# Kernel optimization log

Measured on AMD Instinct MI355X. Metric: run time of the kernel, lower is better.

Reference implementation:

```python
import jax, jax.numpy as jnp
import numpy as np

POLY_DEGREE = 2
EPS = 1e-10
MAX_INTER = 25

# Upper-triangle index pairs (i<j) in the same row-major order as the
# original double loop: (0,1),(0,2),...,(0,24),(1,2),...
_IU0, _IU1 = np.triu_indices(MAX_INTER, k=1)


def setup_inputs() -> dict:
    key = jax.random.key(0)
    x = jax.random.normal(key, (524288, 25), dtype=jnp.float32)
    return {"x": x}


def reference(x) -> jnp.ndarray:
    feats = [x]
    # polynomial features: degrees 2..POLY_DEGREE
    for degree in range(2, POLY_DEGREE + 1):
        feats.append(jnp.power(x, degree))
    ax = jnp.abs(x) + EPS
    feats.append(jnp.log(ax))            # log features
    feats.append(jnp.sqrt(ax))           # sqrt features
    feats.append(jnp.power(ax, 1.0 / 3.0))  # cbrt features
    # pairwise interactions among first min(F,25) columns, upper triangle
    inter = x[:, _IU0] * x[:, _IU1]      # [B, 300]
    feats.append(inter)
    return jnp.concatenate(feats, axis=1)  # [B, 400]
```

## Files before the change

### kernel.cpp

```cpp
#include <hip/hip_runtime.h>

#define NF     25
#define NPAIR  300
#define NUNARY 125
#define NCOL   425
#define ROWS   8
#define BLK    256
#define TILE_DW (ROWS * NCOL)
#define TILE4   (TILE_DW / 4)
#define VALS_N  (ROWS * NF + ROWS * NUNARY + 4)

typedef float f32x4 __attribute__((ext_vector_type(4)));
typedef unsigned int u32;
typedef u32 u32x4 __attribute__((ext_vector_type(4)));

#define ONE_SLOT (ROWS * NF + ROWS * NUNARY)

__global__ __launch_bounds__(BLK) void feat_expand_kernel(
    const float* __restrict__ x, float* __restrict__ out,
    int nrows, int nchunks) {
  __shared__ float vals[VALS_N];
  __shared__ u32x4 dtab4[TILE4];
  u32* dtab = (u32*)dtab4;

  const int tid = threadIdx.x;
  const int r200 = tid / NF;
  const int i200 = tid - r200 * NF;

  if (tid == 0) vals[ONE_SLOT] = 1.0f;
  for (int o = tid; o < TILE_DW; o += BLK) {
    const int r = o / NCOL, c = o - r * NCOL;
    u32 d;
    if (c < NUNARY) {
      d = (u32)(ROWS * NF + r * NUNARY + c) | ((u32)ONE_SLOT << 16);
    } else {
      int rem = c - NUNARY, i = 0;
      while (rem >= (NF - 1 - i)) { rem -= (NF - 1 - i); ++i; }
      const int j = i + 1 + rem;
      d = (u32)(r * NF + i) | ((u32)(r * NF + j) << 16);
    }
    dtab[o] = d;
  }

  for (int chunk = blockIdx.x; chunk < nchunks; chunk += gridDim.x) {
    const long long rowbase = (long long)chunk * ROWS;
    const long long remrows = nrows - rowbase;
    const int rows_here = (int)(remrows < ROWS ? remrows : ROWS);

    __syncthreads();

    if (tid < ROWS * NF && r200 < rows_here) {
      const float v = x[rowbase * NF + tid];
      vals[tid] = v;
      float* ur = &vals[ROWS * NF + r200 * NUNARY];
      const float ax = fabsf(v) + 1e-10f;
      const float l2 = __builtin_amdgcn_logf(ax);
      ur[i200]          = v;
      ur[NF + i200]     = v * v;
      ur[2*NF + i200]   = l2 * 0.69314718055994530942f;
      ur[3*NF + i200]   = sqrtf(ax);
      ur[4*NF + i200]   = __builtin_amdgcn_exp2f(l2 * (1.0f/3.0f));
    }
    __syncthreads();

    if (rows_here == ROWS) {
      f32x4* __restrict__ o4 = (f32x4*)(out + rowbase * NCOL);
#pragma unroll
      for (int k = 0; k < 4; ++k) {
        const int v4 = tid + k * BLK;
        if (k < 3 || v4 < TILE4) {
          const u32x4 d = dtab4[v4];
          f32x4 ov;
          ov.x = vals[d.x & 0xFFFF] * vals[d.x >> 16];
          ov.y = vals[d.y & 0xFFFF] * vals[d.y >> 16];
          ov.z = vals[d.z & 0xFFFF] * vals[d.z >> 16];
          ov.w = vals[d.w & 0xFFFF] * vals[d.w >> 16];
          __builtin_nontemporal_store(ov, &o4[v4]);
        }
      }
    } else {
      const int total = rows_here * NCOL;
      for (int o = tid; o < total; o += BLK) {
        const u32 d = dtab[o];
        out[rowbase * NCOL + o] = vals[d & 0xFFFF] * vals[d >> 16];
      }
    }
  }
}

extern "C" void kernel_launch(void* const* d_in, const int* in_sizes, int n_in,
                              void* d_out, int out_size, void* d_ws, size_t ws_size,
                              hipStream_t stream) {
  const float* x = (const float*)d_in[0];
  float* out = (float*)d_out;

  const int nrows = in_sizes[0] / NF;
  const int nchunks = (nrows + ROWS - 1) / ROWS;
  const int grid = nchunks < 4096 ? nchunks : 4096;

  feat_expand_kernel<<<grid, BLK, 0, stream>>>(x, out, nrows, nchunks);
}
```

Baseline: 214.7 us.

## Give each wavefront its own 4-row chunk to drop block-wide barriers

Each 64-lane wavefront now processes its own 4-row chunk, with a private region of shared memory for input and unary values. Because no data is shared across wavefronts, the two per-iteration __syncthreads are removed and only one barrier remains after the lookup table is built. The aim is to let wavefronts run independently and hide memory latency without block-wide stalls. Correctness now relies on lockstep execution within a wavefront for the shared-memory store-then-load, with no explicit wave barrier. Each wavefront also does fewer stores per input load.

```diff
diff --git a/kernel.cpp b/kernel.cpp
--- a/kernel.cpp
+++ b/kernel.cpp
@@ -1,88 +1,92 @@
 #include <hip/hip_runtime.h>
 
 #define NF     25
-#define NPAIR  300
 #define NUNARY 125
 #define NCOL   425
-#define ROWS   8
+#define WROWS  4
 #define BLK    256
-#define TILE_DW (ROWS * NCOL)
+#define WAVES  (BLK / 64)
+#define WXS    (WROWS * NF)
+#define WVALS  608
+#define ONE_OFF 600
+#define TILE_DW (WROWS * NCOL)
 #define TILE4   (TILE_DW / 4)
-#define VALS_N  (ROWS * NF + ROWS * NUNARY + 4)
 
 typedef float f32x4 __attribute__((ext_vector_type(4)));
 typedef unsigned int u32;
 typedef u32 u32x4 __attribute__((ext_vector_type(4)));
 
-#define ONE_SLOT (ROWS * NF + ROWS * NUNARY)
-
 __global__ __launch_bounds__(BLK) void feat_expand_kernel(
     const float* __restrict__ x, float* __restrict__ out,
-    int nrows, int nchunks) {
-  __shared__ float vals[VALS_N];
+    int nrows, int nwchunks) {
   __shared__ u32x4 dtab4[TILE4];
+  __shared__ float vals[WAVES * WVALS];
   u32* dtab = (u32*)dtab4;
 
-  const int tid = threadIdx.x;
-  const int r200 = tid / NF;
-  const int i200 = tid - r200 * NF;
+  const int tid  = threadIdx.x;
+  const int wid  = tid >> 6;
+  const int lane = tid & 63;
+  float* wv = &vals[wid * WVALS];
 
-  if (tid == 0) vals[ONE_SLOT] = 1.0f;
   for (int o = tid; o < TILE_DW; o += BLK) {
     const int r = o / NCOL, c = o - r * NCOL;
     u32 d;
     if (c < NUNARY) {
-      d = (u32)(ROWS * NF + r * NUNARY + c) | ((u32)ONE_SLOT << 16);
+      d = (u32)(WXS + r * NUNARY + c) | ((u32)ONE_OFF << 16);
     } else {
       int rem = c - NUNARY, i = 0;
       while (rem >= (NF - 1 - i)) { rem -= (NF - 1 - i); ++i; }
-      const int j = i + 1 + rem;
-      d = (u32)(r * NF + i) | ((u32)(r * NF + j) << 16);
+      d = (u32)(r * NF + i) | ((u32)(r * NF + i + 1 + rem) << 16);
     }
     dtab[o] = d;
   }
+  if (lane == 0) wv[ONE_OFF] = 1.0f;
+  __syncthreads();
 
-  for (int chunk = blockIdx.x; chunk < nchunks; chunk += gridDim.x) {
-    const long long rowbase = (long long)chunk * ROWS;
-    const long long remrows = nrows - rowbase;
-    const int rows_here = (int)(remrows < ROWS ? remrows : ROWS);
+  const int gwaves = gridDim.x * WAVES;
+  for (int wc = blockIdx.x * WAVES + wid; wc < nwchunks; wc += gwaves) {
+    const long long rowbase = (long long)wc * WROWS;
+    const long long remr = nrows - rowbase;
+    const int rows_here = (int)(remr < WROWS ? remr : WROWS);
 
-    __syncthreads();
+#pragma unroll
+    for (int k = 0; k < 2; ++k) {
+      const int idx = lane + k * 64;
+      const int r = idx / NF, i = idx - r * NF;
+      if (idx < WXS && r < rows_here) {
+        const float v = x[rowbase * NF + idx];
+        wv[idx] = v;
+        float* ur = &wv[WXS + r * NUNARY];
+        const float ax = fabsf(v) + 1e-10f;
+        const float l2 = __builtin_amdgcn_logf(ax);
+        ur[i]          = v;
+        ur[NF + i]     = v * v;
+        ur[2*NF + i]   = l2 * 0.69314718055994530942f;
+        ur[3*NF + i]   = sqrtf(ax);
+        ur[4*NF + i]   = __builtin_amdgcn_exp2f(l2 * (1.0f/3.0f));
+      }
+    }
 
-    if (tid < ROWS * NF && r200 < rows_here) {
-      const float v = x[rowbase * NF + tid];
-      vals[tid] = v;
-      float* ur = &vals[ROWS * NF + r200 * NUNARY];
-      const float ax = fabsf(v) + 1e-10f;
-      const float l2 = __builtin_amdgcn_logf(ax);
-      ur[i200]          = v;
-      ur[NF + i200]     = v * v;
-      ur[2*NF + i200]   = l2 * 0.69314718055994530942f;
-      ur[3*NF + i200]   = sqrtf(ax);
-      ur[4*NF + i200]   = __builtin_amdgcn_exp2f(l2 * (1.0f/3.0f));
-    }
-    __syncthreads();
-
-    if (rows_here == ROWS) {
-      f32x4* __restrict__ o4 = (f32x4*)(out + rowbase * NCOL);
+    if (rows_here == WROWS) {
+      f32x4* o4 = (f32x4*)(out + rowbase * NCOL);
 #pragma unroll
-      for (int k = 0; k < 4; ++k) {
-        const int v4 = tid + k * BLK;
-        if (k < 3 || v4 < TILE4) {
+      for (int k = 0; k < 7; ++k) {
+        const int v4 = lane + k * 64;
+        if (k < 6 || v4 < TILE4) {
           const u32x4 d = dtab4[v4];
           f32x4 ov;
-          ov.x = vals[d.x & 0xFFFF] * vals[d.x >> 16];
-          ov.y = vals[d.y & 0xFFFF] * vals[d.y >> 16];
-          ov.z = vals[d.z & 0xFFFF] * vals[d.z >> 16];
-          ov.w = vals[d.w & 0xFFFF] * vals[d.w >> 16];
+          ov.x = wv[d.x & 0xFFFF] * wv[d.x >> 16];
+          ov.y = wv[d.y & 0xFFFF] * wv[d.y >> 16];
+          ov.z = wv[d.z & 0xFFFF] * wv[d.z >> 16];
+          ov.w = wv[d.w & 0xFFFF] * wv[d.w >> 16];
           __builtin_nontemporal_store(ov, &o4[v4]);
         }
       }
     } else {
       const int total = rows_here * NCOL;
-      for (int o = tid; o < total; o += BLK) {
+      for (int o = lane; o < total; o += 64) {
         const u32 d = dtab[o];
-        out[rowbase * NCOL + o] = vals[d & 0xFFFF] * vals[d >> 16];
+        out[rowbase * NCOL + o] = wv[d & 0xFFFF] * wv[d >> 16];
       }
     }
   }
@@ -95,8 +99,9 @@
   float* out = (float*)d_out;
 
   const int nrows = in_sizes[0] / NF;
-  const int nchunks = (nrows + ROWS - 1) / ROWS;
-  const int grid = nchunks < 4096 ? nchunks : 4096;
+  const int nwchunks = (nrows + WROWS - 1) / WROWS;
+  const int nblocks = (nwchunks + WAVES - 1) / WAVES;
+  const int grid = nblocks < 4096 ? nblocks : 4096;
 
-  feat_expand_kernel<<<grid, BLK, 0, stream>>>(x, out, nrows, nchunks);
+  feat_expand_kernel<<<grid, BLK, 0, stream>>>(x, out, nrows, nwchunks);
 }
```

After: 224.1 us. +4.4%, slower.

## Keep gather descriptors in registers and double rows per chunk

Applied to the files above, without the earlier changes.

The per-block shared-memory descriptor table is replaced by descriptors computed once into per-thread registers, which removes one LDS vector load per output quad. Each chunk now covers 16 rows instead of 8, so all threads take part in the unary-feature stage (two passes) and each barrier pair is spread over more output. Launch bounds now request 6 blocks per CU. The cost is around 28 descriptor registers per thread and a slower tail path that recomputes indices on the fly.

```diff
diff --git a/kernel.cpp b/kernel.cpp
--- a/kernel.cpp
+++ b/kernel.cpp
@@ -4,85 +4,103 @@
 #define NPAIR  300
 #define NUNARY 125
 #define NCOL   425
-#define ROWS   8
+#define ROWS   16
 #define BLK    256
+#define LOADN   (ROWS * NF)
+#define NVALS   (LOADN + ROWS * NUNARY + 1)
+#define ONE_SLOT (LOADN + ROWS * NUNARY)
 #define TILE_DW (ROWS * NCOL)
-#define TILE4   (TILE_DW / 4)
-#define VALS_N  (ROWS * NF + ROWS * NUNARY + 4)
+#define TILE4N  (TILE_DW / 4)
+#define C4FULL  (TILE4N / BLK)
+#define C4REM   (TILE4N - C4FULL * BLK)
 
 typedef float f32x4 __attribute__((ext_vector_type(4)));
 typedef unsigned int u32;
-typedef u32 u32x4 __attribute__((ext_vector_type(4)));
 
-#define ONE_SLOT (ROWS * NF + ROWS * NUNARY)
-
-__global__ __launch_bounds__(BLK) void feat_expand_kernel(
+__global__ __launch_bounds__(BLK, 6) void feat_expand_kernel(
     const float* __restrict__ x, float* __restrict__ out,
     int nrows, int nchunks) {
-  __shared__ float vals[VALS_N];
-  __shared__ u32x4 dtab4[TILE4];
-  u32* dtab = (u32*)dtab4;
+  __shared__ float vals[NVALS];
 
   const int tid = threadIdx.x;
-  const int r200 = tid / NF;
-  const int i200 = tid - r200 * NF;
+
+  u32 dsc[(C4FULL + 1) * 4];
+#pragma unroll
+  for (int k = 0; k <= C4FULL; ++k) {
+#pragma unroll
+    for (int e = 0; e < 4; ++e) {
+      int o = 4 * (tid + k * BLK) + e;
+      if (o >= TILE_DW) o = 0;
+      const int r = o / NCOL, c = o - r * NCOL;
+      u32 d;
+      if (c < NUNARY) {
+        d = (u32)(LOADN + r * NUNARY + c) | ((u32)ONE_SLOT << 16);
+      } else {
+        int rem = c - NUNARY, i = 0;
+        while (rem >= (NF - 1 - i)) { rem -= (NF - 1 - i); ++i; }
+        d = (u32)(r * NF + i) | ((u32)(r * NF + i + 1 + rem) << 16);
+      }
+      dsc[k * 4 + e] = d;
+    }
+  }
 
   if (tid == 0) vals[ONE_SLOT] = 1.0f;
-  for (int o = tid; o < TILE_DW; o += BLK) {
-    const int r = o / NCOL, c = o - r * NCOL;
-    u32 d;
-    if (c < NUNARY) {
-      d = (u32)(ROWS * NF + r * NUNARY + c) | ((u32)ONE_SLOT << 16);
-    } else {
-      int rem = c - NUNARY, i = 0;
-      while (rem >= (NF - 1 - i)) { rem -= (NF - 1 - i); ++i; }
-      const int j = i + 1 + rem;
-      d = (u32)(r * NF + i) | ((u32)(r * NF + j) << 16);
-    }
-    dtab[o] = d;
-  }
 
-  for (int chunk = blockIdx.x; chunk < nchunks; chunk += gridDim.x) {
-    const long long rowbase = (long long)chunk * ROWS;
-    const long long remrows = nrows - rowbase;
-    const int rows_here = (int)(remrows < ROWS ? remrows : ROWS);
+  for (long long chunk = blockIdx.x; chunk < nchunks; chunk += gridDim.x) {
+    const long long rowbase = chunk * ROWS;
+    const long long remr = nrows - rowbase;
+    const int rows_here = (int)(remr < ROWS ? remr : ROWS);
 
     __syncthreads();
 
-    if (tid < ROWS * NF && r200 < rows_here) {
-      const float v = x[rowbase * NF + tid];
-      vals[tid] = v;
-      float* ur = &vals[ROWS * NF + r200 * NUNARY];
-      const float ax = fabsf(v) + 1e-10f;
-      const float l2 = __builtin_amdgcn_logf(ax);
-      ur[i200]          = v;
-      ur[NF + i200]     = v * v;
-      ur[2*NF + i200]   = l2 * 0.69314718055994530942f;
-      ur[3*NF + i200]   = sqrtf(ax);
-      ur[4*NF + i200]   = __builtin_amdgcn_exp2f(l2 * (1.0f/3.0f));
+#pragma unroll
+    for (int k = 0; k < 2; ++k) {
+      const int idx = tid + k * BLK;
+      if (idx < LOADN) {
+        const int r = idx / NF, i = idx - r * NF;
+        float v = 0.0f;
+        if (r < rows_here) v = x[rowbase * NF + idx];
+        vals[idx] = v;
+        float* ur = &vals[LOADN + r * NUNARY];
+        const float ax = fabsf(v) + 1e-10f;
+        const float l2 = __builtin_amdgcn_logf(ax);
+        ur[i]          = v;
+        ur[NF + i]     = v * v;
+        ur[2*NF + i]   = l2 * 0.69314718055994530942f;
+        ur[3*NF + i]   = sqrtf(ax);
+        ur[4*NF + i]   = __builtin_amdgcn_exp2f(l2 * (1.0f/3.0f));
+      }
     }
     __syncthreads();
 
     if (rows_here == ROWS) {
       f32x4* __restrict__ o4 = (f32x4*)(out + rowbase * NCOL);
 #pragma unroll
-      for (int k = 0; k < 4; ++k) {
+      for (int k = 0; k <= C4FULL; ++k) {
         const int v4 = tid + k * BLK;
-        if (k < 3 || v4 < TILE4) {
-          const u32x4 d = dtab4[v4];
+        if (k < C4FULL || tid < C4REM) {
+          const u32 d0 = dsc[4*k], d1 = dsc[4*k+1], d2 = dsc[4*k+2], d3 = dsc[4*k+3];
           f32x4 ov;
-          ov.x = vals[d.x & 0xFFFF] * vals[d.x >> 16];
-          ov.y = vals[d.y & 0xFFFF] * vals[d.y >> 16];
-          ov.z = vals[d.z & 0xFFFF] * vals[d.z >> 16];
-          ov.w = vals[d.w & 0xFFFF] * vals[d.w >> 16];
+          ov.x = vals[d0 & 0xFFFF] * vals[d0 >> 16];
+          ov.y = vals[d1 & 0xFFFF] * vals[d1 >> 16];
+          ov.z = vals[d2 & 0xFFFF] * vals[d2 >> 16];
+          ov.w = vals[d3 & 0xFFFF] * vals[d3 >> 16];
           __builtin_nontemporal_store(ov, &o4[v4]);
         }
       }
     } else {
       const int total = rows_here * NCOL;
       for (int o = tid; o < total; o += BLK) {
-        const u32 d = dtab[o];
-        out[rowbase * NCOL + o] = vals[d & 0xFFFF] * vals[d >> 16];
+        const int r = o / NCOL, c = o - r * NCOL;
+        float vv;
+        if (c < NUNARY) {
+          vv = vals[LOADN + r * NUNARY + c];
+        } else {
+          int rem2 = c - NUNARY, i = 0;
+          while (rem2 >= (NF - 1 - i)) { rem2 -= (NF - 1 - i); ++i; }
+          vv = vals[r * NF + i] * vals[r * NF + i + 1 + rem2];
+        }
+        out[rowbase * NCOL + o] = vv;
       }
     }
   }
```

Measured after the change: 205.4 us. 4.3% less time.
